# Performance work log

Measured on AMD Instinct MI355X. Metric: run time of the kernel, lower is better.

## Reference

```python
import jax, jax.numpy as jnp
import numpy as np

DEPTH = 4
EPS = 1e-5


def _bn(x, g, b):
    # training-mode BatchNorm over (B,H,W) per channel
    m = x.mean(axis=(0, 2, 3), keepdims=True)
    v = x.var(axis=(0, 2, 3), keepdims=True)
    return (x - m) * jax.lax.rsqrt(v + EPS) * g[None, :, None, None] + b[None, :, None, None]


def _conv_bn(x, w, g, b):
    # 1x1 conv (no bias) + BatchNorm
    y = jnp.einsum('bchw,oc->bohw', x, w)
    return _bn(y, g, b)


def _block_max_broadcast(x, gsz):
    # max over each (H/gsz, W/gsz) block of a gsz x gsz grid, broadcast back
    B, C, H, W = x.shape
    xr = x.reshape(B, C, gsz, H // gsz, gsz, W // gsz)
    m = xr.max(axis=(3, 5), keepdims=True)
    return jnp.broadcast_to(m, xr.shape).reshape(B, C, H, W)


def setup_inputs() -> dict:
    key = jax.random.key(0)
    ks = jax.random.split(key, 3)
    B, C, H, W = 4, 128, 256, 256
    x = jax.random.normal(ks[0], (B, C, H, W), dtype=jnp.float32)
    conv_w = jax.random.normal(ks[1], (DEPTH, C, C), dtype=jnp.float32) * 0.05
    conv_g = jnp.ones((DEPTH, C), dtype=jnp.float32)
    conv_b = jnp.zeros((DEPTH, C), dtype=jnp.float32)
    final_w = jax.random.normal(ks[2], (C, (DEPTH + 1) * C), dtype=jnp.float32) * 0.05
    final_g = jnp.ones((C,), dtype=jnp.float32)
    final_b = jnp.zeros((C,), dtype=jnp.float32)
    return {"x": x, "conv_w": conv_w, "conv_g": conv_g, "conv_b": conv_b,
            "final_w": final_w, "final_g": final_g, "final_b": final_b}


def reference(x, conv_w, conv_g, conv_b, final_w, final_g, final_b):
    # p[0]: identity; p[1+d]: block-max over 2^d x 2^d grid broadcast back, then 1x1 conv+BN
    p = [x]
    for d in range(DEPTH):
        pooled = _block_max_broadcast(x, 2 ** d)  # d=0 -> global max broadcast
        p.append(_conv_bn(pooled, conv_w[d], conv_g[d], conv_b[d]))
    out = jnp.concatenate(p, axis=1)  # [B, 5C, H, W]
    return _conv_bn(out, final_w, final_g, final_b)
```

## Files before the change

### kernel.cpp

```cpp
#include <hip/hip_runtime.h>
#include <hip/hip_bf16.h>
#include <math.h>
#include <float.h>

#define B_ 4
#define C_ 128
#define P_ 65536

#define M3_OFF      0
#define M2_OFF      32768
#define M1_OFF      40960
#define M0_OFF      43008
#define YBASE_      43520
#define SCALED_OFF  87040
#define SHIFTD_OFF  87552
#define CONTRIB_OFF 88064
#define S3_OFF      120832
#define SX_OFF      153600
#define G_OFF       154112
#define SCALEF_OFF  219648
#define SHIFTF_OFF  219776
#define MAXP_OFF    219904
#define SUMP_OFF    744192

using short8 = __attribute__((ext_vector_type(8))) short;
using f32x4 = __attribute__((ext_vector_type(4))) float;

__device__ __forceinline__ int level_rel(int d) {
    return YBASE_ - 512 * (((1 << (2 * (d + 1))) - 1) / 3);
}

__device__ __forceinline__ unsigned int bfpair(float a, float b) {
    unsigned int ua = __float_as_uint(a), ub = __float_as_uint(b);
    ua = (ua + 0x7fffu + ((ua >> 16) & 1u)) >> 16;
    ub = (ub + 0x7fffu + ((ub >> 16) & 1u)) & 0xffff0000u;
    return ua | ub;
}

__global__ __launch_bounds__(256) void k_gram_pool(const float* __restrict__ x,
                                                   float* __restrict__ ws,
                                                   float* __restrict__ gpart) {
    __shared__ uint4 tileq[2048];
    unsigned char* tile = (unsigned char*)tileq;
    int wg = blockIdx.x;
    int b = wg >> 7, rc = wg & 127;
    const float* xb = x + (size_t)b * C_ * P_ + (size_t)rc * 512;
    int t = threadIdx.x, l = t & 63, wv = t >> 6;
    int pq = t & 31, ci = t >> 5;

    f32x4 acc[2][8];
#pragma unroll
    for (int i = 0; i < 2; ++i)
#pragma unroll
        for (int j = 0; j < 8; ++j) acc[i][j] = (f32x4){0.f, 0.f, 0.f, 0.f};
    float mx[16][2], sm[16][2];
#pragma unroll
    for (int k = 0; k < 16; ++k)
#pragma unroll
        for (int par = 0; par < 2; ++par) { mx[k][par] = -FLT_MAX; sm[k][par] = 0.f; }

#pragma unroll
    for (int s = 0; s < 4; ++s) {
#pragma unroll
        for (int k = 0; k < 16; ++k) {
            int c = ci + 8 * k;
            float4 v = *(const float4*)(xb + (size_t)c * P_ + s * 128 + pq * 4);
            mx[k][s & 1] = fmaxf(mx[k][s & 1],
                                 fmaxf(fmaxf(v.x, v.y), fmaxf(v.z, v.w)));
            sm[k][s & 1] += (v.x + v.y) + (v.z + v.w);
            unsigned int u0 = bfpair(v.x, v.y), u1 = bfpair(v.z, v.w);
            int wa = (c * 256 + pq * 8) ^ ((c & 7) << 4);
            *(uint2*)(tile + wa) = make_uint2(u0, u1);
        }
        __syncthreads();
#pragma unroll
        for (int ks = 0; ks < 4; ++ks) {
            int col = ks * 64 + (l >> 4) * 16;
            int ra0 = (((2 * wv) * 16 + (l & 15)) * 256 + col) ^ ((l & 7) << 4);
            int ra1 = (((2 * wv + 1) * 16 + (l & 15)) * 256 + col) ^ ((l & 7) << 4);
            short8 a0 = *(const short8*)(tile + ra0);
            short8 a1 = *(const short8*)(tile + ra1);
#pragma unroll
            for (int nt = 0; nt < 8; ++nt) {
                int rb = ((nt * 16 + (l & 15)) * 256 + col) ^ ((l & 7) << 4);
                short8 bb = *(const short8*)(tile + rb);
                acc[0][nt] = __builtin_amdgcn_mfma_f32_16x16x32_bf16(a0, bb, acc[0][nt], 0, 0, 0);
                acc[1][nt] = __builtin_amdgcn_mfma_f32_16x16x32_bf16(a1, bb, acc[1][nt], 0, 0, 0);
            }
        }
        __syncthreads();
    }
    size_t gb = (size_t)wg * 16384;
#pragma unroll
    for (int mt2 = 0; mt2 < 2; ++mt2) {
        int mt = wv * 2 + mt2;
#pragma unroll
        for (int nt = 0; nt < 8; ++nt)
#pragma unroll
            for (int r = 0; r < 4; ++r)
                gpart[gb + (size_t)(mt * 16 + (l >> 4) * 4 + r) * 128 + nt * 16 + (l & 15)] =
                    acc[mt2][nt][r];
    }
    int i3 = rc >> 4, rr = rc & 15;
#pragma unroll
    for (int k = 0; k < 16; ++k)
#pragma unroll
        for (int par = 0; par < 2; ++par) {
            float m = mx[k][par], s2 = sm[k][par];
            m = fmaxf(m, __shfl_xor(m, 1)); s2 += __shfl_xor(s2, 1);
            m = fmaxf(m, __shfl_xor(m, 2)); s2 += __shfl_xor(s2, 2);
            m = fmaxf(m, __shfl_xor(m, 4)); s2 += __shfl_xor(s2, 4);
            if ((pq & 7) == 0) {
                int c = ci + 8 * k;
                int j3 = par * 4 + (pq >> 3);
                size_t idx = ((size_t)(b * 128 + c) * 64 + i3 * 8 + j3) * 16 + rr;
                ws[MAXP_OFF + idx] = m;
                ws[SUMP_OFF + idx] = s2;
            }
        }
}

__global__ __launch_bounds__(256) void k_reduceG(const float* __restrict__ gpart,
                                                 float* __restrict__ ws) {
    int tid = blockIdx.x * 256 + threadIdx.x;
    int b = tid >> 14, inner = tid & 16383;
    const float* p = gpart + (size_t)b * 128 * 16384 + inner;
    float s = 0.f;
    for (int r = 0; r < 128; ++r) s += p[(size_t)r * 16384];
    ws[G_OFF + tid] = s;
}

__global__ __launch_bounds__(256) void k_reduceMS(float* __restrict__ ws) {
    int bc = blockIdx.x;
    int t = threadIdx.x;
    int blk = t >> 2, q = t & 3;
    __shared__ float bm[64], bs[64];
    __shared__ float lv[24];
    __shared__ float sxr[8];
    {
        size_t base = (size_t)bc * 1024 + blk * 16 + q * 4;
        float4 mv = *(const float4*)(ws + MAXP_OFF + base);
        float4 sv = *(const float4*)(ws + SUMP_OFF + base);
        float m = fmaxf(fmaxf(mv.x, mv.y), fmaxf(mv.z, mv.w));
        float s = (sv.x + sv.y) + (sv.z + sv.w);
        m = fmaxf(m, __shfl_xor(m, 1)); s += __shfl_xor(s, 1);
        m = fmaxf(m, __shfl_xor(m, 2)); s += __shfl_xor(s, 2);
        if (q == 0) {
            bm[blk] = m;
            bs[blk] = s;
            ws[M3_OFF + (size_t)bc * 64 + blk] = m;
            ws[S3_OFF + (size_t)bc * 64 + blk] = s;
        }
    }
    __syncthreads();
    if (t < 8) {
        float sx = 0.f;
        for (int r = 0; r < 8; ++r) sx += bs[t * 8 + r];
        sxr[t] = sx;
    }
    if (t < 16) {
        int i2 = t >> 2, j2 = t & 3;
        float m = -FLT_MAX;
        for (int a = 0; a < 2; ++a)
            for (int b2 = 0; b2 < 2; ++b2)
                m = fmaxf(m, bm[(2 * i2 + a) * 8 + 2 * j2 + b2]);
        lv[t] = m;
        ws[M2_OFF + (size_t)bc * 16 + t] = m;
    }
    __syncthreads();
    if (t == 0) {
        float sx = 0.f;
        for (int r = 0; r < 8; ++r) sx += sxr[r];
        ws[SX_OFF + bc] = sx;
    }
    if (t < 4) {
        int i1 = t >> 1, j1 = t & 1;
        float m = -FLT_MAX;
        for (int a = 0; a < 2; ++a)
            for (int b2 = 0; b2 < 2; ++b2)
                m = fmaxf(m, lv[(2 * i1 + a) * 4 + 2 * j1 + b2]);
        lv[16 + t] = m;
        ws[M1_OFF + (size_t)bc * 4 + t] = m;
    }
    __syncthreads();
    if (t == 0)
        ws[M0_OFF + bc] = fmaxf(fmaxf(lv[16], lv[17]), fmaxf(lv[18], lv[19]));
}

__global__ __launch_bounds__(256) void k_conv_pool(const float* __restrict__ conv_w,
                                                   float* __restrict__ ws) {
    int bid = blockIdx.x;
    int d = bid >> 4, b = (bid >> 2) & 3, cchunk = bid & 3;
    int NB = 1 << (2 * d);
    int rel = level_rel(d);
    const float* Mb = ws + rel + (size_t)b * 128 * NB;
    float* Yb = ws + YBASE_ + rel + (size_t)b * 128 * NB;
    __shared__ float mlds[8192];
    int t = threadIdx.x;
    int tot = 128 * NB;
    for (int i = t; i < tot; i += 256) mlds[i] = Mb[i];
    __syncthreads();
    if (NB >= 4) {
        int nbq = NB >> 2;
        int nq = 32 * nbq;
        for (int qi = t; qi < nq; qi += 256) {
            int co = cchunk * 32 + (qi >> (2 * d - 2));
            int bq = qi & (nbq - 1);
            const float* wrow = conv_w + ((size_t)d * 128 + co) * 128;
            float a0 = 0.f, a1 = 0.f, a2 = 0.f, a3 = 0.f;
            for (int ci = 0; ci < 128; ++ci) {
                float4 mv = *(const float4*)(&mlds[ci * NB + bq * 4]);
                float wvv = wrow[ci];
                a0 = fmaf(wvv, mv.x, a0);
                a1 = fmaf(wvv, mv.y, a1);
                a2 = fmaf(wvv, mv.z, a2);
                a3 = fmaf(wvv, mv.w, a3);
            }
            float4 r;
            r.x = a0; r.y = a1; r.z = a2; r.w = a3;
            *(float4*)(&Yb[co * NB + bq * 4]) = r;
        }
    } else {
        for (int oi = t; oi < 32; oi += 256) {
            int co = cchunk * 32 + oi;
            const float* wrow = conv_w + (size_t)co * 128;
            float acc = 0.f;
            for (int ci = 0; ci < 128; ++ci) acc = fmaf(mlds[ci], wrow[ci], acc);
            Yb[co] = acc;
        }
    }
}

__global__ __launch_bounds__(256) void k_bnstats_d(const float* __restrict__ conv_g,
                                                   const float* __restrict__ conv_b,
                                                   float* __restrict__ ws) {
    int tid = blockIdx.x * 256 + threadIdx.x;
    if (tid >= 512) return;
    int d = tid >> 7, c = tid & 127;
    int NB = 1 << (2 * d);
    const float* Y = ws + YBASE_ + level_rel(d);
    int n = 4 * NB;
    float s = 0.f;
    for (int b = 0; b < 4; ++b)
        for (int k = 0; k < NB; ++k) s += Y[((size_t)b * 128 + c) * NB + k];
    float mean = s / (float)n;
    float v = 0.f;
    for (int b = 0; b < 4; ++b)
        for (int k = 0; k < NB; ++k) {
            float dd = Y[((size_t)b * 128 + c) * NB + k] - mean;
            v = fmaf(dd, dd, v);
        }
    float var = v / (float)n;
    float sc = conv_g[d * 128 + c] * rsqrtf(var + 1e-5f);
    ws[SCALED_OFF + tid] = sc;
    ws[SHIFTD_OFF + tid] = conv_b[d * 128 + c] - mean * sc;
}

__global__ __launch_bounds__(128) void k_contrib(const float* __restrict__ final_w,
                                                 float* __restrict__ ws) {
    int b = blockIdx.x >> 6, blk3 = blockIdx.x & 63;
    int i3 = blk3 >> 3, j3 = blk3 & 7;
    __shared__ float pn[512];
    int t = threadIdx.x;
    for (int k = t; k < 512; k += 128) {
        int d = k >> 7, c = k & 127;
        int sh = 3 - d;
        int blkd = (i3 >> sh) * (1 << d) + (j3 >> sh);
        int NB = 1 << (2 * d);
        float yv = ws[YBASE_ + level_rel(d) + ((size_t)b * 128 + c) * NB + blkd];
        pn[k] = yv * ws[SCALED_OFF + k] + ws[SHIFTD_OFF + k];
    }
    __syncthreads();
    const float* fw = final_w + (size_t)t * 640 + 128;
    float acc = 0.f;
#pragma unroll 8
    for (int k = 0; k < 512; k += 4) {
        float4 f = *(const float4*)(fw + k);
        acc = fmaf(pn[k], f.x, acc);
        acc = fmaf(pn[k + 1], f.y, acc);
        acc = fmaf(pn[k + 2], f.z, acc);
        acc = fmaf(pn[k + 3], f.w, acc);
    }
    ws[CONTRIB_OFF + ((size_t)b * 128 + t) * 64 + blk3] = acc;
}

__global__ __launch_bounds__(128) void k_stats(const float* __restrict__ final_w,
                                               const float* __restrict__ final_g,
                                               const float* __restrict__ final_b,
                                               float* __restrict__ ws) {
    int o = blockIdx.x, t = threadIdx.x;
    __shared__ __align__(16) float wlds[128];
    __shared__ __align__(16) float cvl[64];
    __shared__ float rbuf[4];
    wlds[t] = final_w[(size_t)o * 640 + t];
    __syncthreads();
    float SSQ = 0.f, SUM = 0.f;
    for (int b = 0; b < 4; ++b) {
        if (t < 64) cvl[t] = ws[CONTRIB_OFF + (size_t)(b * 128 + o) * 64 + t];
        __syncthreads();
        const float* Gb = ws + G_OFF + (size_t)b * 16384 + (size_t)t * 128;
        float a1 = 0.f;
#pragma unroll 8
        for (int k = 0; k < 128; k += 4) {
            float4 g = *(const float4*)(Gb + k);
            float4 w = *(const float4*)(&wlds[k]);
            a1 = fmaf(g.x, w.x, fmaf(g.y, w.y, fmaf(g.z, w.z, fmaf(g.w, w.w, a1))));
        }
        const float* S3p = ws + S3_OFF + (size_t)(b * 128 + t) * 64;
        float a2 = 0.f;
#pragma unroll 8
        for (int k = 0; k < 64; k += 4) {
            float4 sv = *(const float4*)(S3p + k);
            float4 cv = *(const float4*)(&cvl[k]);
            a2 = fmaf(sv.x, cv.x, fmaf(sv.y, cv.y, fmaf(sv.z, cv.z, fmaf(sv.w, cv.w, a2))));
        }
        float r1 = (a1 + 2.f * a2) * wlds[t];
        float r2 = wlds[t] * ws[SX_OFF + b * 128 + t];
        if (t < 64) {
            r1 += 1024.f * cvl[t] * cvl[t];
            r2 += 1024.f * cvl[t];
        }
#pragma unroll
        for (int k = 1; k < 64; k <<= 1) {
            r1 += __shfl_xor(r1, k);
            r2 += __shfl_xor(r2, k);
        }
        if ((t & 63) == 0) {
            rbuf[(t >> 6) * 2] = r1;
            rbuf[(t >> 6) * 2 + 1] = r2;
        }
        __syncthreads();
        SSQ += rbuf[0] + rbuf[2];
        SUM += rbuf[1] + rbuf[3];
        __syncthreads();
    }
    if (t == 0) {
        float mean = SUM / 262144.f;
        float var = SSQ / 262144.f - mean * mean;
        float sc = final_g[o] * rsqrtf(var + 1e-5f);
        ws[SCALEF_OFF + o] = sc;
        ws[SHIFTF_OFF + o] = final_b[o] - mean * sc;
    }
}

__global__ __launch_bounds__(256) void k_out(const float* __restrict__ x,
                                             const float* __restrict__ final_w,
                                             const float* __restrict__ ws,
                                             float* __restrict__ out) {
    __shared__ uint4 wtileq[2048];
    __shared__ float scl[128], shf[128], cvs[512];
    unsigned char* wtile = (unsigned char*)wtileq;
    int wgid = blockIdx.x;
    int b = wgid >> 9, pt = wgid & 511;
    int p0 = pt * 128;
    int t = threadIdx.x, l = t & 63, wv = t >> 6;
#pragma unroll
    for (int it = 0; it < 32; ++it) {
        int pid = it * 256 + t;
        int o = pid >> 6, cp = (pid & 63) * 2;
        float2 f = *(const float2*)(final_w + (size_t)o * 640 + cp);
        unsigned int u = bfpair(f.x, f.y);
        int wa = (o * 256 + cp * 2) ^ ((o & 7) << 4);
        *(unsigned int*)(wtile + wa) = u;
    }
    if (t < 128) {
        scl[t] = ws[SCALEF_OFF + t];
        shf[t] = ws[SHIFTF_OFF + t];
    }
    int i3 = pt >> 6, jb = (pt & 1) * 4;
    for (int q = t; q < 512; q += 256) {
        int o = q >> 2, jj = q & 3;
        cvs[q] = ws[CONTRIB_OFF + (size_t)(b * 128 + o) * 64 + i3 * 8 + jb + jj];
    }
    __syncthreads();

    const float* xb = x + (size_t)b * C_ * P_;
    int pw = p0 + wv * 32;
    f32x4 acc[8][2];
#pragma unroll
    for (int i = 0; i < 8; ++i) {
        acc[i][0] = (f32x4){0.f, 0.f, 0.f, 0.f};
        acc[i][1] = (f32x4){0.f, 0.f, 0.f, 0.f};
    }
#pragma unroll
    for (int ks = 0; ks < 4; ++ks) {
        short8 bf[2];
#pragma unroll
        for (int nt = 0; nt < 2; ++nt) {
            const float* xp = xb + (size_t)(ks * 32 + (l >> 4) * 8) * P_ + (pw + nt * 16 + (l & 15));
            float f0 = xp[0 * P_], f1 = xp[1 * P_], f2 = xp[2 * P_], f3 = xp[3 * P_];
            float f4 = xp[4 * P_], f5 = xp[5 * P_], f6 = xp[6 * P_], f7 = xp[7 * P_];
            union { uint4 u; short8 s; } cvtu;
            cvtu.u = make_uint4(bfpair(f0, f1), bfpair(f2, f3), bfpair(f4, f5), bfpair(f6, f7));
            bf[nt] = cvtu.s;
        }
#pragma unroll
        for (int mt = 0; mt < 8; ++mt) {
            int ra = ((mt * 16 + (l & 15)) * 256 + ks * 64 + (l >> 4) * 16) ^ ((l & 7) << 4);
            short8 af = *(const short8*)(wtile + ra);
            acc[mt][0] = __builtin_amdgcn_mfma_f32_16x16x32_bf16(af, bf[0], acc[mt][0], 0, 0, 0);
            acc[mt][1] = __builtin_amdgcn_mfma_f32_16x16x32_bf16(af, bf[1], acc[mt][1], 0, 0, 0);
        }
    }
#pragma unroll
    for (int mt = 0; mt < 8; ++mt)
#pragma unroll
        for (int nt = 0; nt < 2; ++nt) {
            int p = pw + nt * 16 + (l & 15);
            int jj = ((p & 255) >> 5) & 3;
#pragma unroll
            for (int r = 0; r < 4; ++r) {
                int o = mt * 16 + (l >> 4) * 4 + r;
                float z = acc[mt][nt][r] + cvs[o * 4 + jj];
                out[(size_t)(b * 128 + o) * P_ + p] = fmaf(z, scl[o], shf[o]);
            }
        }
}

extern "C" void kernel_launch(void* const* d_in, const int* in_sizes, int n_in,
                              void* d_out, int out_size, void* d_ws, size_t ws_size,
                              hipStream_t stream) {
    const float* x = (const float*)d_in[0];
    const float* conv_w = (const float*)d_in[1];
    const float* conv_g = (const float*)d_in[2];
    const float* conv_b = (const float*)d_in[3];
    const float* final_w = (const float*)d_in[4];
    const float* final_g = (const float*)d_in[5];
    const float* final_b = (const float*)d_in[6];
    float* out = (float*)d_out;
    float* ws = (float*)d_ws;

    k_gram_pool<<<512, 256, 0, stream>>>(x, ws, out);
    k_reduceG<<<256, 256, 0, stream>>>(out, ws);
    k_reduceMS<<<512, 256, 0, stream>>>(ws);
    k_conv_pool<<<64, 256, 0, stream>>>(conv_w, ws);
    k_bnstats_d<<<2, 256, 0, stream>>>(conv_g, conv_b, ws);
    k_contrib<<<B_ * 64, 128, 0, stream>>>(final_w, ws);
    k_stats<<<128, 128, 0, stream>>>(final_w, final_g, final_b, ws);
    k_out<<<2048, 256, 0, stream>>>(x, final_w, ws, out);
}
```

Before: 209.3 us.

## Load x tiles via direct global-to-LDS copies and use 32x32 MFMA tiles

The gram/pool kernel now streams fp32 x tiles straight into shared memory with global_load_lds, skipping the per-thread register round trip and bf16 packing at store time. Max and sum pooling are computed by reading the fp32 tile back from LDS. Fragments are converted to bf16 when loaded from LDS. The matmul switches from 16x16x32 to 32x32x16 MFMA with a 2x2 per-wave tile for more operand reuse. LDS use grows from 32KB to 64KB, which may lower occupancy, and the bf16 conversion is now repeated on every fragment load.

```diff
diff --git a/kernel.cpp b/kernel.cpp
--- a/kernel.cpp
+++ b/kernel.cpp
@@ -25,6 +25,7 @@
 
 using short8 = __attribute__((ext_vector_type(8))) short;
 using f32x4 = __attribute__((ext_vector_type(4))) float;
+using f32x16 = __attribute__((ext_vector_type(16))) float;
 
 __device__ __forceinline__ int level_rel(int d) {
     return YBASE_ - 512 * (((1 << (2 * (d + 1))) - 1) / 3);
@@ -37,86 +38,118 @@
     return ua | ub;
 }
 
+#define GLDS16(src, dst)                                                    \
+    __builtin_amdgcn_global_load_lds(                                       \
+        (const __attribute__((address_space(1))) unsigned int*)(src),       \
+        (__attribute__((address_space(3))) unsigned int*)(dst), 16, 0, 0)
+
+__device__ __forceinline__ short8 ld_frag(const float* tile, int row, int ks, int l) {
+    int ch = ks * 4 + ((l >> 5) << 1);
+    int sw = row & 7;
+    const float* p0 = tile + row * 128 + ((ch ^ sw) << 2);
+    const float* p1 = tile + row * 128 + (((ch + 1) ^ sw) << 2);
+    float4 v0 = *(const float4*)p0;
+    float4 v1 = *(const float4*)p1;
+    union { uint4 u; short8 s; } cu;
+    cu.u = make_uint4(bfpair(v0.x, v0.y), bfpair(v0.z, v0.w),
+                      bfpair(v1.x, v1.y), bfpair(v1.z, v1.w));
+    return cu.s;
+}
+
 __global__ __launch_bounds__(256) void k_gram_pool(const float* __restrict__ x,
                                                    float* __restrict__ ws,
                                                    float* __restrict__ gpart) {
-    __shared__ uint4 tileq[2048];
-    unsigned char* tile = (unsigned char*)tileq;
+    __shared__ float tile[16384];
     int wg = blockIdx.x;
     int b = wg >> 7, rc = wg & 127;
     const float* xb = x + (size_t)b * C_ * P_ + (size_t)rc * 512;
     int t = threadIdx.x, l = t & 63, wv = t >> 6;
-    int pq = t & 31, ci = t >> 5;
-
-    f32x4 acc[2][8];
+    int rhalf = l >> 5;
+    int lchunk = l & 31;
+    int tc = t >> 2, tjb = t & 3;
+
+    int tr = (wv >> 1) * 64;
+    int tcc = (wv & 1) * 64;
+
+    f32x16 acc[2][2];
 #pragma unroll
     for (int i = 0; i < 2; ++i)
 #pragma unroll
-        for (int j = 0; j < 8; ++j) acc[i][j] = (f32x4){0.f, 0.f, 0.f, 0.f};
-    float mx[16][2], sm[16][2];
-#pragma unroll
-    for (int k = 0; k < 16; ++k)
-#pragma unroll
-        for (int par = 0; par < 2; ++par) { mx[k][par] = -FLT_MAX; sm[k][par] = 0.f; }
+        for (int j = 0; j < 2; ++j)
+#pragma unroll
+            for (int r = 0; r < 16; ++r) acc[i][j][r] = 0.f;
+    float mx[2][2], sm[2][2];
+#pragma unroll
+    for (int i = 0; i < 2; ++i)
+#pragma unroll
+        for (int j = 0; j < 2; ++j) { mx[i][j] = -FLT_MAX; sm[i][j] = 0.f; }
 
 #pragma unroll
     for (int s = 0; s < 4; ++s) {
 #pragma unroll
-        for (int k = 0; k < 16; ++k) {
-            int c = ci + 8 * k;
-            float4 v = *(const float4*)(xb + (size_t)c * P_ + s * 128 + pq * 4);
-            mx[k][s & 1] = fmaxf(mx[k][s & 1],
-                                 fmaxf(fmaxf(v.x, v.y), fmaxf(v.z, v.w)));
-            sm[k][s & 1] += (v.x + v.y) + (v.z + v.w);
-            unsigned int u0 = bfpair(v.x, v.y), u1 = bfpair(v.z, v.w);
-            int wa = (c * 256 + pq * 8) ^ ((c & 7) << 4);
-            *(uint2*)(tile + wa) = make_uint2(u0, u1);
+        for (int i = 0; i < 16; ++i) {
+            int c = wv * 32 + i * 2;
+            int row = c + rhalf;
+            int chunk = lchunk ^ (row & 7);
+            GLDS16(xb + (size_t)row * P_ + s * 128 + chunk * 4, &tile[c * 128]);
         }
         __syncthreads();
-#pragma unroll
-        for (int ks = 0; ks < 4; ++ks) {
-            int col = ks * 64 + (l >> 4) * 16;
-            int ra0 = (((2 * wv) * 16 + (l & 15)) * 256 + col) ^ ((l & 7) << 4);
-            int ra1 = (((2 * wv + 1) * 16 + (l & 15)) * 256 + col) ^ ((l & 7) << 4);
-            short8 a0 = *(const short8*)(tile + ra0);
-            short8 a1 = *(const short8*)(tile + ra1);
-#pragma unroll
-            for (int nt = 0; nt < 8; ++nt) {
-                int rb = ((nt * 16 + (l & 15)) * 256 + col) ^ ((l & 7) << 4);
-                short8 bb = *(const short8*)(tile + rb);
-                acc[0][nt] = __builtin_amdgcn_mfma_f32_16x16x32_bf16(a0, bb, acc[0][nt], 0, 0, 0);
-                acc[1][nt] = __builtin_amdgcn_mfma_f32_16x16x32_bf16(a1, bb, acc[1][nt], 0, 0, 0);
+
+#pragma unroll
+        for (int ci2 = 0; ci2 < 2; ++ci2) {
+            int c = tc + ci2 * 64;
+            float m = -FLT_MAX, sum = 0.f;
+#pragma unroll
+            for (int k = 0; k < 8; ++k) {
+                int phys = (tjb * 8 + k) ^ (c & 7);
+                float4 v = *(const float4*)(tile + c * 128 + phys * 4);
+                m = fmaxf(m, fmaxf(fmaxf(v.x, v.y), fmaxf(v.z, v.w)));
+                sum += (v.x + v.y) + (v.z + v.w);
             }
+            if ((s & 1) == 0) {
+                mx[0][ci2] = fmaxf(mx[0][ci2], m);
+                sm[0][ci2] += sum;
+            } else {
+                mx[1][ci2] = fmaxf(mx[1][ci2], m);
+                sm[1][ci2] += sum;
+            }
+        }
+
+#pragma unroll
+        for (int ks = 0; ks < 8; ++ks) {
+            short8 af0 = ld_frag(tile, tr + (l & 31), ks, l);
+            short8 af1 = ld_frag(tile, tr + 32 + (l & 31), ks, l);
+            short8 bf0 = ld_frag(tile, tcc + (l & 31), ks, l);
+            short8 bf1 = ld_frag(tile, tcc + 32 + (l & 31), ks, l);
+            acc[0][0] = __builtin_amdgcn_mfma_f32_32x32x16_bf16(af0, bf0, acc[0][0], 0, 0, 0);
+            acc[0][1] = __builtin_amdgcn_mfma_f32_32x32x16_bf16(af0, bf1, acc[0][1], 0, 0, 0);
+            acc[1][0] = __builtin_amdgcn_mfma_f32_32x32x16_bf16(af1, bf0, acc[1][0], 0, 0, 0);
+            acc[1][1] = __builtin_amdgcn_mfma_f32_32x32x16_bf16(af1, bf1, acc[1][1], 0, 0, 0);
         }
         __syncthreads();
     }
+
     size_t gb = (size_t)wg * 16384;
 #pragma unroll
-    for (int mt2 = 0; mt2 < 2; ++mt2) {
-        int mt = wv * 2 + mt2;
-#pragma unroll
-        for (int nt = 0; nt < 8; ++nt)
-#pragma unroll
-            for (int r = 0; r < 4; ++r)
-                gpart[gb + (size_t)(mt * 16 + (l >> 4) * 4 + r) * 128 + nt * 16 + (l & 15)] =
-                    acc[mt2][nt][r];
-    }
+    for (int i = 0; i < 2; ++i)
+#pragma unroll
+        for (int j = 0; j < 2; ++j)
+#pragma unroll
+            for (int r = 0; r < 16; ++r) {
+                int row = tr + i * 32 + (r & 3) + 8 * (r >> 2) + 4 * (l >> 5);
+                int col = tcc + j * 32 + (l & 31);
+                gpart[gb + (size_t)row * 128 + col] = acc[i][j][r];
+            }
     int i3 = rc >> 4, rr = rc & 15;
 #pragma unroll
-    for (int k = 0; k < 16; ++k)
-#pragma unroll
-        for (int par = 0; par < 2; ++par) {
-            float m = mx[k][par], s2 = sm[k][par];
-            m = fmaxf(m, __shfl_xor(m, 1)); s2 += __shfl_xor(s2, 1);
-            m = fmaxf(m, __shfl_xor(m, 2)); s2 += __shfl_xor(s2, 2);
-            m = fmaxf(m, __shfl_xor(m, 4)); s2 += __shfl_xor(s2, 4);
-            if ((pq & 7) == 0) {
-                int c = ci + 8 * k;
-                int j3 = par * 4 + (pq >> 3);
-                size_t idx = ((size_t)(b * 128 + c) * 64 + i3 * 8 + j3) * 16 + rr;
-                ws[MAXP_OFF + idx] = m;
-                ws[SUMP_OFF + idx] = s2;
-            }
+    for (int sp = 0; sp < 2; ++sp)
+#pragma unroll
+        for (int ci2 = 0; ci2 < 2; ++ci2) {
+            int c = tc + ci2 * 64;
+            int j3 = sp * 4 + tjb;
+            size_t idx = ((size_t)(b * 128 + c) * 64 + i3 * 8 + j3) * 16 + rr;
+            ws[MAXP_OFF + idx] = mx[sp][ci2];
+            ws[SUMP_OFF + idx] = sm[sp][ci2];
         }
 }
 
```

New measurement: 211.0 us. Within noise of the previous version (+0.8%).
